# Kernel optimization log

Hardware: AMD Instinct MI355X
Metric: run time of the kernel (lower is better)

Reference implementation:

```python
import jax, jax.numpy as jnp
import numpy as np

B, T, D, H = 4, 2048, 1024, 16
HD = D // H
EPS = 1e-5
NEG = 1e10


def setup_inputs() -> dict:
    key = jax.random.key(0)
    k1, k2, k3 = jax.random.split(key, 3)
    return {
        "target": jax.random.normal(k1, (B, T, D), dtype=jnp.float32),
        "w_qkv": jax.random.normal(k2, (D, 3 * D), dtype=jnp.float32) * 0.02,
        "w_proj": jax.random.normal(k3, (D, D), dtype=jnp.float32) * (0.02 / np.sqrt(24.0)),
        "b_proj": jnp.zeros((D,), dtype=jnp.float32),
        "ln_gamma": jnp.ones((D,), dtype=jnp.float32),
        "ln_beta": jnp.zeros((D,), dtype=jnp.float32),
    }


def reference(target, w_qkv, w_proj, b_proj, ln_gamma, ln_beta):
    b, t, d = target.shape
    resid = target
    qkv = target @ w_qkv                      # [B,T,3D]
    q, k, v = jnp.split(qkv, 3, axis=-1)
    # [B,H,T,hd]
    q = q.reshape(b, t, H, HD).transpose(0, 2, 1, 3)
    k = k.reshape(b, t, H, HD).transpose(0, 2, 1, 3)
    v = v.reshape(b, t, H, HD).transpose(0, 2, 1, 3)
    scores = jnp.einsum("bhqd,bhkd->bhqk", q, k) * (1.0 / np.sqrt(HD))
    causal = (jnp.arange(t)[:, None] >= jnp.arange(t)[None, :]).astype(scores.dtype)
    scores = scores * causal - (1.0 - causal) * NEG
    attn = jax.nn.softmax(scores, axis=-1)
    out = jnp.einsum("bhqk,bhkd->bhqd", attn, v)
    out = out.transpose(0, 2, 1, 3).reshape(b, t, d)
    proj = out @ w_proj + b_proj
    x = proj + resid
    mu = jnp.mean(x, axis=-1, keepdims=True)
    var = jnp.var(x, axis=-1, keepdims=True)
    return ((x - mu) * jax.lax.rsqrt(var + EPS)) * ln_gamma + ln_beta
```

## Files before the change

kernel.cpp:

```cpp
#include <hip/hip_runtime.h>
#include <hip/hip_bf16.h>

#define Bsz 4
#define Tseq 2048
#define Dmodel 1024
#define Hn 16
#define HD 64
#define EPS 1e-5f
#define QSCALE 0.18033688011112042f

typedef __attribute__((ext_vector_type(8))) short bf16x8;
typedef __attribute__((ext_vector_type(4))) short bf16x4;
typedef __attribute__((ext_vector_type(4))) float f32x4;
typedef __attribute__((ext_vector_type(4))) unsigned short us4;
typedef __attribute__((ext_vector_type(2))) unsigned uint2v;

typedef const __attribute__((address_space(1))) void* gas_t;
typedef __attribute__((address_space(3))) void* las_t;

__device__ __forceinline__ unsigned short f2bf(float x) {
    unsigned u = __builtin_bit_cast(unsigned, x);
    u += 0x7fffu + ((u >> 16) & 1u);
    return (unsigned short)(u >> 16);
}
__device__ __forceinline__ unsigned pack2bf_t(float a, float b) {
    return __builtin_amdgcn_perm(__builtin_bit_cast(unsigned, b),
                                 __builtin_bit_cast(unsigned, a), 0x07060302u);
}

__device__ __forceinline__ float exp2_raw(float x) {
#if __has_builtin(__builtin_amdgcn_exp2f)
    return __builtin_amdgcn_exp2f(x);
#else
    float r;
    asm("v_exp_f32 %0, %1" : "=v"(r) : "v"(x));
    return r;
#endif
}

__device__ __forceinline__ f32x4 mfma16x16x16(bf16x4 a, bf16x4 b, f32x4 c) {
#if __has_builtin(__builtin_amdgcn_mfma_f32_16x16x16bf16_1k)
    return __builtin_amdgcn_mfma_f32_16x16x16bf16_1k(a, b, c, 0, 0, 0);
#else
    asm("v_mfma_f32_16x16x16_bf16 %0, %1, %2, %0" : "+v"(c) : "v"(a), "v"(b));
    return c;
#endif
}

__global__ __launch_bounds__(256)
void prep(const float* __restrict__ target, unsigned short* __restrict__ tgt_bf,
          const float* __restrict__ w_qkv, unsigned short* __restrict__ wqT,
          const float* __restrict__ w_proj, unsigned short* __restrict__ wpT) {
    const int bid = blockIdx.x;
    const int tid = threadIdx.x;
    if (bid < 8192) {
        int i = (bid * 256 + tid) * 4;
        float4 v = *(const float4*)(target + i);
        us4 o = { f2bf(v.x), f2bf(v.y), f2bf(v.z), f2bf(v.w) };
        *(us4*)(tgt_bf + i) = o;
        return;
    }
    __shared__ unsigned short t[32][33];
    const float* in;
    unsigned short* outp;
    int K = 1024, N, bx, by;
    if (bid < 8192 + 3072) {
        const int b2 = bid - 8192;
        in = w_qkv; outp = wqT; N = 3072;
        bx = b2 % 96; by = b2 / 96;
    } else {
        const int b3 = bid - 8192 - 3072;
        in = w_proj; outp = wpT; N = 1024;
        bx = b3 & 31; by = b3 >> 5;
    }
    const int k0 = by * 32, n0 = bx * 32;
    const int tx = tid & 31, ty = tid >> 5;
    #pragma unroll
    for (int i = 0; i < 32; i += 8)
        t[ty + i][tx] = f2bf(in[(size_t)(k0 + ty + i) * N + n0 + tx]);
    __syncthreads();
    #pragma unroll
    for (int i = 0; i < 32; i += 8)
        outp[(size_t)(n0 + ty + i) * K + k0 + tx] = t[tx][ty + i];
}

template<bool OUT_BF16, bool SCALEQ>
__global__ __launch_bounds__(256)
void gemm_mfma(const unsigned short* __restrict__ A,
               const unsigned short* __restrict__ Bt,
               void* __restrict__ Cv, int M, int N, int K,
               const float* __restrict__ bias, const float* __restrict__ resid) {
    __shared__ unsigned short As[2][128 * 32];
    __shared__ unsigned short Bs[2][128 * 32];
    const int tid = threadIdx.x;
    const int w = tid >> 6, lane = tid & 63;
    const int l16 = lane & 15, quad = lane >> 4;

    const int lin = blockIdx.y * gridDim.x + blockIdx.x;
    const int chunk = (gridDim.x * gridDim.y) >> 3;
    const int neff = (lin & 7) * chunk + (lin >> 3);
    const int bx = neff % gridDim.x, by = neff / gridDim.x;
    const int m0 = by * 128, n0 = bx * 128;

    f32x4 acc[4][4];
    #pragma unroll
    for (int i = 0; i < 4; ++i)
        #pragma unroll
        for (int j = 0; j < 4; ++j)
            acc[i][j] = f32x4{0.f, 0.f, 0.f, 0.f};

    const int lrow = lane >> 2, lcol = lane & 3;
    const unsigned short* ag = A  + (size_t)(m0 + w * 32 + lrow) * K + lcol * 8;
    const unsigned short* bg = Bt + (size_t)(n0 + w * 32 + lrow) * K + lcol * 8;
    unsigned short* al0 = As[0] + (w * 32) * 32;
    unsigned short* al1 = As[0] + (w * 32 + 16) * 32;
    unsigned short* ah0 = As[1] + (w * 32) * 32;
    unsigned short* ah1 = As[1] + (w * 32 + 16) * 32;
    unsigned short* bl0 = Bs[0] + (w * 32) * 32;
    unsigned short* bl1 = Bs[0] + (w * 32 + 16) * 32;
    unsigned short* bh0 = Bs[1] + (w * 32) * 32;
    unsigned short* bh1 = Bs[1] + (w * 32 + 16) * 32;
    const int am = (w >> 1) * 64, bn = (w & 1) * 64;

    for (int k0 = 0; k0 < K; k0 += 64) {
        __builtin_amdgcn_global_load_lds((gas_t)(ag + k0),               (las_t)al0, 16, 0, 0);
        __builtin_amdgcn_global_load_lds((gas_t)(ag + 16 * K + k0),      (las_t)al1, 16, 0, 0);
        __builtin_amdgcn_global_load_lds((gas_t)(ag + k0 + 32),          (las_t)ah0, 16, 0, 0);
        __builtin_amdgcn_global_load_lds((gas_t)(ag + 16 * K + k0 + 32), (las_t)ah1, 16, 0, 0);
        __builtin_amdgcn_global_load_lds((gas_t)(bg + k0),               (las_t)bl0, 16, 0, 0);
        __builtin_amdgcn_global_load_lds((gas_t)(bg + 16 * K + k0),      (las_t)bl1, 16, 0, 0);
        __builtin_amdgcn_global_load_lds((gas_t)(bg + k0 + 32),          (las_t)bh0, 16, 0, 0);
        __builtin_amdgcn_global_load_lds((gas_t)(bg + 16 * K + k0 + 32), (las_t)bh1, 16, 0, 0);
        __syncthreads();

        #pragma unroll
        for (int ks = 0; ks < 2; ++ks) {
            bf16x8 af[4], bf[4];
            #pragma unroll
            for (int i = 0; i < 4; ++i)
                af[i] = *(const bf16x8*)&As[ks][(am + i * 16 + l16) * 32 + quad * 8];
            #pragma unroll
            for (int j = 0; j < 4; ++j)
                bf[j] = *(const bf16x8*)&Bs[ks][(bn + j * 16 + l16) * 32 + quad * 8];
            #pragma unroll
            for (int i = 0; i < 4; ++i)
                #pragma unroll
                for (int j = 0; j < 4; ++j)
                    acc[i][j] = __builtin_amdgcn_mfma_f32_16x16x32_bf16(af[i], bf[j], acc[i][j], 0, 0, 0);
        }
        __syncthreads();
    }

    #pragma unroll
    for (int i = 0; i < 4; ++i) {
        #pragma unroll
        for (int j = 0; j < 4; ++j) {
            const int col = n0 + bn + j * 16 + l16;
            const float scale = (SCALEQ && col < Dmodel) ? QSCALE : 1.0f;
            #pragma unroll
            for (int r = 0; r < 4; ++r) {
                const int row = m0 + am + i * 16 + quad * 4 + r;
                if (OUT_BF16) {
                    ((unsigned short*)Cv)[(size_t)row * N + col] = f2bf(acc[i][j][r] * scale);
                } else {
                    float v = acc[i][j][r] + bias[col] + resid[(size_t)row * N + col];
                    ((float*)Cv)[(size_t)row * N + col] = v;
                }
            }
        }
    }
}

__global__ __launch_bounds__(256)
void flash_attn(const unsigned short* __restrict__ qkv, unsigned short* __restrict__ out) {
    const int lin = blockIdx.y * gridDim.x + blockIdx.x;
    const int xcd = lin & 7, local = lin >> 3;
    const int bh = xcd + 8 * (local & 7);
    const int x = local >> 3;
    const int qt_lo = x, qt_hi = (Tseq / 64 - 1) - x;
    const int h = bh & (Hn - 1), b = bh >> 4;
    const int tid = threadIdx.x;
    const int wave = tid >> 6;
    const int lane = tid & 63;
    const int l16 = lane & 15;
    const int quad = lane >> 4;

    __shared__ unsigned short Ks[2][2][64 * 32];
    __shared__ unsigned short Vs[2][64 * 64];

    const unsigned short* qrow = qkv + ((size_t)(b * Tseq + wave * 16 + l16)) * 3072 + h * HD;
    const unsigned short* qhi = qrow + (size_t)qt_hi * 64 * 3072;
    const unsigned short* qlo = qrow + (size_t)qt_lo * 64 * 3072;
    bf16x8 qh0 = *(const bf16x8*)(qhi + quad * 8);
    bf16x8 qh1 = *(const bf16x8*)(qhi + 32 + quad * 8);
    bf16x8 ql0 = *(const bf16x8*)(qlo + quad * 8);
    bf16x8 ql1 = *(const bf16x8*)(qlo + 32 + quad * 8);

    f32x4 lacc_hi = {0.f, 0.f, 0.f, 0.f}, lacc_lo = {0.f, 0.f, 0.f, 0.f};
    f32x4 ohi[4], olo[4];
    #pragma unroll
    for (int nt = 0; nt < 4; ++nt) {
        ohi[nt] = f32x4{0.f, 0.f, 0.f, 0.f};
        olo[nt] = f32x4{0.f, 0.f, 0.f, 0.f};
    }
    const bf16x4 vones = { (short)0x3F80, (short)0x3F80, (short)0x3F80, (short)0x3F80 };

    unsigned vrb[4];
    #pragma unroll
    for (int ntd = 0; ntd < 4; ++ntd) {
        const int d = ntd * 16 + l16;
        const int X = (d + (d >> 3)) & 7;
        vrb[ntd] = (unsigned)(d * 128 + (quad & 1) * 8)
                 ^ (unsigned)(X << 4) ^ (unsigned)((quad >> 1) << 4);
    }

    const unsigned short* kbase = qkv + (size_t)b * Tseq * 3072 + Dmodel + h * HD;
    const unsigned short* vbase = kbase + Dmodel;
    const unsigned short* kg = kbase + (size_t)(wave * 16 + (lane >> 2)) * 3072 + (lane & 3) * 8;
    const int vp = tid >> 3, vc = tid & 7;
    const unsigned short* vsrc = vbase + (size_t)(2 * vp) * 3072 + vc * 8;

    auto stageK = [&](int buf, size_t koff) {
        __builtin_amdgcn_global_load_lds((gas_t)(kg + koff),
                                         (las_t)&Ks[buf][0][wave * 16 * 32], 16, 0, 0);
        __builtin_amdgcn_global_load_lds((gas_t)(kg + koff + 32),
                                         (las_t)&Ks[buf][1][wave * 16 * 32], 16, 0, 0);
    };
    auto writeV = [&](int buf, const bf16x8& va, const bf16x8& vb) {
        const int kc = vp >> 2;
        const int kin = (2 * vp) & 7;
        #pragma unroll
        for (int j = 0; j < 8; ++j) {
            const int d = vc * 8 + j;
            const int pc = kc ^ ((d + (d >> 3)) & 7);
            unsigned pk = (unsigned)(unsigned short)va[j]
                        | ((unsigned)(unsigned short)vb[j] << 16);
            *(unsigned*)&Vs[buf][d * 64 + pc * 8 + kin] = pk;
        }
    };

    auto compute = [&](int buf, int q0t, const bf16x8& qf0, const bf16x8& qf1,
                       f32x4* oacc, f32x4& lacc, bool diag, int k0g) {
        __builtin_amdgcn_s_setprio(1);
        f32x4 st[4];
        #pragma unroll
        for (int nt = 0; nt < 4; ++nt) {
            f32x4 a = {0.f, 0.f, 0.f, 0.f};
            bf16x8 kf0 = *(const bf16x8*)&Ks[buf][0][(nt * 16 + l16) * 32 + quad * 8];
            a = __builtin_amdgcn_mfma_f32_16x16x32_bf16(kf0, qf0, a, 0, 0, 0);
            bf16x8 kf1 = *(const bf16x8*)&Ks[buf][1][(nt * 16 + l16) * 32 + quad * 8];
            a = __builtin_amdgcn_mfma_f32_16x16x32_bf16(kf1, qf1, a, 0, 0, 0);
            st[nt] = a;
        }
        if (diag) {
            const int qg = q0t + wave * 16 + l16;
            #pragma unroll
            for (int nt = 0; nt < 4; ++nt) {
                const int kgl = k0g + nt * 16 + quad * 4;
                #pragma unroll
                for (int r = 0; r < 4; ++r)
                    if (kgl + r > qg) st[nt][r] = -1e30f;
            }
        }
        bf16x4 pa[4];
        #pragma unroll
        for (int nt = 0; nt < 4; ++nt) {
            float p0 = exp2_raw(st[nt][0]);
            float p1 = exp2_raw(st[nt][1]);
            float p2 = exp2_raw(st[nt][2]);
            float p3 = exp2_raw(st[nt][3]);
            uint2v t;
            t.x = pack2bf_t(p0, p1);
            t.y = pack2bf_t(p2, p3);
            pa[nt] = __builtin_bit_cast(bf16x4, t);
        }
        const char* vsb = (const char*)&Vs[buf][0];
        #pragma unroll
        for (int ntk = 0; ntk < 4; ++ntk) {
            lacc = mfma16x16x16(pa[ntk], vones, lacc);
            #pragma unroll
            for (int ntd = 0; ntd < 4; ++ntd) {
                bf16x4 vf = *(const bf16x4*)(vsb + (vrb[ntd] ^ (unsigned)(ntk << 5)));
                oacc[ntd] = mfma16x16x16(pa[ntk], vf, oacc[ntd]);
            }
        }
        __builtin_amdgcn_s_setprio(0);
    };

    stageK(0, 0);
    bf16x8 va = *(const bf16x8*)(vsrc);
    bf16x8 vb = *(const bf16x8*)(vsrc + 3072);
    writeV(0, va, vb);
    __syncthreads();

    int cur = 0;
    for (int kt = 0; kt <= qt_hi; ++kt) {
        if (kt < qt_hi) {
            const size_t koff_n = (size_t)(kt + 1) * 64 * 3072;
            stageK(cur ^ 1, koff_n);
            va = *(const bf16x8*)(vsrc + koff_n);
            vb = *(const bf16x8*)(vsrc + koff_n + 3072);
        }

        compute(cur, qt_hi * 64, qh0, qh1, ohi, lacc_hi, kt == qt_hi, kt * 64);
        if (kt <= qt_lo)
            compute(cur, qt_lo * 64, ql0, ql1, olo, lacc_lo, kt == qt_lo, kt * 64);

        if (kt < qt_hi) writeV(cur ^ 1, va, vb);
        __syncthreads();
        cur ^= 1;
    }

    auto epilogue = [&](int q0t, f32x4* oacc, const f32x4& lacc) {
        float inv[4];
        #pragma unroll
        for (int r = 0; r < 4; ++r)
            inv[r] = __builtin_amdgcn_rcpf(lacc[r]);
        unsigned short* obase =
            out + ((size_t)(b * Tseq + q0t + wave * 16)) * Dmodel + h * HD;
        #pragma unroll
        for (int nt = 0; nt < 4; ++nt) {
            #pragma unroll
            for (int r = 0; r < 4; ++r) {
                int row = quad * 4 + r;
                obase[(size_t)row * Dmodel + nt * 16 + l16] = f2bf(oacc[nt][r] * inv[r]);
            }
        }
    };
    epilogue(qt_hi * 64, ohi, lacc_hi);
    epilogue(qt_lo * 64, olo, lacc_lo);
}

__global__ __launch_bounds__(256)
void ln_kernel(float* __restrict__ x, const float* __restrict__ gamma,
               const float* __restrict__ beta) {
    const int row = blockIdx.x;
    float* xr = x + (size_t)row * Dmodel;
    const int tid = threadIdx.x;
    const int wave = tid >> 6;
    __shared__ float ws[4], ws2[4];

    float4 v = *(const float4*)(xr + tid * 4);
    float s  = v.x + v.y + v.z + v.w;
    float s2 = v.x * v.x + v.y * v.y + v.z * v.z + v.w * v.w;
    #pragma unroll
    for (int off = 32; off; off >>= 1) {
        s  += __shfl_xor(s, off, 64);
        s2 += __shfl_xor(s2, off, 64);
    }
    if ((tid & 63) == 0) { ws[wave] = s; ws2[wave] = s2; }
    __syncthreads();
    s  = (ws[0] + ws[1]) + (ws[2] + ws[3]);
    s2 = (ws2[0] + ws2[1]) + (ws2[2] + ws2[3]);

    const float mu  = s * (1.0f / Dmodel);
    const float var = s2 * (1.0f / Dmodel) - mu * mu;
    const float rstd = rsqrtf(var + EPS);

    float4 g = *(const float4*)(gamma + tid * 4);
    float4 bt = *(const float4*)(beta + tid * 4);
    float4 o;
    o.x = (v.x - mu) * rstd * g.x + bt.x;
    o.y = (v.y - mu) * rstd * g.y + bt.y;
    o.z = (v.z - mu) * rstd * g.z + bt.z;
    o.w = (v.w - mu) * rstd * g.w + bt.w;
    *(float4*)(xr + tid * 4) = o;
}

extern "C" void kernel_launch(void* const* d_in, const int* in_sizes, int n_in,
                              void* d_out, int out_size, void* d_ws, size_t ws_size,
                              hipStream_t stream) {
    const float* target   = (const float*)d_in[0];
    const float* w_qkv    = (const float*)d_in[1];
    const float* w_proj   = (const float*)d_in[2];
    const float* b_proj   = (const float*)d_in[3];
    const float* ln_gamma = (const float*)d_in[4];
    const float* ln_beta  = (const float*)d_in[5];
    float* out = (float*)d_out;

    const int M = Bsz * Tseq;

    char* ws = (char*)d_ws;
    unsigned short* qkv_bf16 = (unsigned short*)(ws);
    unsigned short* attn_bf  = (unsigned short*)(ws + 48ull * 1024 * 1024);
    unsigned short* tgt_bf   = (unsigned short*)(ws + 64ull * 1024 * 1024);
    unsigned short* wqT      = (unsigned short*)(ws + 80ull * 1024 * 1024);
    unsigned short* wpT      = (unsigned short*)(ws + 86ull * 1024 * 1024);

    prep<<<dim3(8192 + 3072 + 1024), 256, 0, stream>>>(
        target, tgt_bf, w_qkv, wqT, w_proj, wpT);

    gemm_mfma<true, true><<<dim3(3072 / 128, M / 128), 256, 0, stream>>>(
        tgt_bf, wqT, qkv_bf16, M, 3072, Dmodel, nullptr, nullptr);

    flash_attn<<<dim3(16, Bsz * Hn), 256, 0, stream>>>(qkv_bf16, attn_bf);

    gemm_mfma<false, false><<<dim3(Dmodel / 128, M / 128), 256, 0, stream>>>(
        attn_bf, wpT, out, M, Dmodel, Dmodel, b_proj, target);

    ln_kernel<<<dim3(M), 256, 0, stream>>>(out, ln_gamma, ln_beta);
}
```

Before: 273.5 us.

## Fuse dual-query-tile attention compute and widen V transpose stores to 64-bit

Merges the two per-tile compute calls into one dual pass, so each K and V fragment read from LDS feeds both the high and low query tiles and their MFMAs can interleave. The V staging is reorganised so each thread loads four rows of four columns and writes 64-bit packed transposed chunks instead of eight 32-bit stores. The intent is to cut redundant LDS reads and store instructions and to raise MFMA ILP. The cost is higher register pressure from holding two sets of P fragments at once. It also assumes qt_hi is never below qt_lo, since the dual branch applies no causal mask to the high tile.

```diff
diff --git a/kernel.cpp b/kernel.cpp
--- a/kernel.cpp
+++ b/kernel.cpp
@@ -26,6 +26,11 @@
 __device__ __forceinline__ unsigned pack2bf_t(float a, float b) {
     return __builtin_amdgcn_perm(__builtin_bit_cast(unsigned, b),
                                  __builtin_bit_cast(unsigned, a), 0x07060302u);
+}
+__device__ __forceinline__ unsigned pack_sel(uint2v a, uint2v b, int j) {
+    unsigned ad = a[j >> 1], bd = b[j >> 1];
+    return (j & 1) ? __builtin_amdgcn_perm(bd, ad, 0x07060302u)
+                   : __builtin_amdgcn_perm(bd, ad, 0x05040100u);
 }
 
 __device__ __forceinline__ float exp2_raw(float x) {
@@ -217,8 +222,8 @@
     const unsigned short* kbase = qkv + (size_t)b * Tseq * 3072 + Dmodel + h * HD;
     const unsigned short* vbase = kbase + Dmodel;
     const unsigned short* kg = kbase + (size_t)(wave * 16 + (lane >> 2)) * 3072 + (lane & 3) * 8;
-    const int vp = tid >> 3, vc = tid & 7;
-    const unsigned short* vsrc = vbase + (size_t)(2 * vp) * 3072 + vc * 8;
+    const int kq = tid >> 4, dq = tid & 15;
+    const unsigned short* vsrc = vbase + (size_t)(4 * kq) * 3072 + dq * 4;
 
     auto stageK = [&](int buf, size_t koff) {
         __builtin_amdgcn_global_load_lds((gas_t)(kg + koff),
@@ -226,71 +231,86 @@
         __builtin_amdgcn_global_load_lds((gas_t)(kg + koff + 32),
                                          (las_t)&Ks[buf][1][wave * 16 * 32], 16, 0, 0);
     };
-    auto writeV = [&](int buf, const bf16x8& va, const bf16x8& vb) {
-        const int kc = vp >> 2;
-        const int kin = (2 * vp) & 7;
-        #pragma unroll
-        for (int j = 0; j < 8; ++j) {
-            const int d = vc * 8 + j;
+    auto loadV = [&](size_t koff, uint2v* v4) {
+        const unsigned short* vr = vsrc + koff;
+        v4[0] = *(const uint2v*)(vr);
+        v4[1] = *(const uint2v*)(vr + 3072);
+        v4[2] = *(const uint2v*)(vr + 2 * 3072);
+        v4[3] = *(const uint2v*)(vr + 3 * 3072);
+    };
+    auto writeV = [&](int buf, const uint2v* v4) {
+        const int kc = kq >> 1;
+        const int kin = (kq & 1) * 4;
+        #pragma unroll
+        for (int j = 0; j < 4; ++j) {
+            const int d = dq * 4 + j;
             const int pc = kc ^ ((d + (d >> 3)) & 7);
-            unsigned pk = (unsigned)(unsigned short)va[j]
-                        | ((unsigned)(unsigned short)vb[j] << 16);
-            *(unsigned*)&Vs[buf][d * 64 + pc * 8 + kin] = pk;
+            uint2v wv;
+            wv.x = pack_sel(v4[0], v4[1], j);
+            wv.y = pack_sel(v4[2], v4[3], j);
+            *(uint2v*)&Vs[buf][d * 64 + pc * 8 + kin] = wv;
         }
     };
 
-    auto compute = [&](int buf, int q0t, const bf16x8& qf0, const bf16x8& qf1,
-                       f32x4* oacc, f32x4& lacc, bool diag, int k0g) {
+    auto computeDual = [&](int buf, bool dual, bool diag_hi, bool diag_lo, int k0g)
+            __attribute__((always_inline)) {
         __builtin_amdgcn_s_setprio(1);
-        f32x4 st[4];
+        bf16x4 pah[4], pal[4];
+        const int qg_hi = qt_hi * 64 + wave * 16 + l16;
+        const int qg_lo = qt_lo * 64 + wave * 16 + l16;
         #pragma unroll
         for (int nt = 0; nt < 4; ++nt) {
-            f32x4 a = {0.f, 0.f, 0.f, 0.f};
             bf16x8 kf0 = *(const bf16x8*)&Ks[buf][0][(nt * 16 + l16) * 32 + quad * 8];
-            a = __builtin_amdgcn_mfma_f32_16x16x32_bf16(kf0, qf0, a, 0, 0, 0);
             bf16x8 kf1 = *(const bf16x8*)&Ks[buf][1][(nt * 16 + l16) * 32 + quad * 8];
-            a = __builtin_amdgcn_mfma_f32_16x16x32_bf16(kf1, qf1, a, 0, 0, 0);
-            st[nt] = a;
-        }
-        if (diag) {
-            const int qg = q0t + wave * 16 + l16;
-            #pragma unroll
-            for (int nt = 0; nt < 4; ++nt) {
-                const int kgl = k0g + nt * 16 + quad * 4;
-                #pragma unroll
-                for (int r = 0; r < 4; ++r)
-                    if (kgl + r > qg) st[nt][r] = -1e30f;
+            const int kgl = k0g + nt * 16 + quad * 4;
+            {
+                f32x4 a = {0.f, 0.f, 0.f, 0.f};
+                a = __builtin_amdgcn_mfma_f32_16x16x32_bf16(kf0, qh0, a, 0, 0, 0);
+                a = __builtin_amdgcn_mfma_f32_16x16x32_bf16(kf1, qh1, a, 0, 0, 0);
+                if (diag_hi) {
+                    #pragma unroll
+                    for (int r = 0; r < 4; ++r)
+                        if (kgl + r > qg_hi) a[r] = -1e30f;
+                }
+                uint2v t;
+                t.x = pack2bf_t(exp2_raw(a[0]), exp2_raw(a[1]));
+                t.y = pack2bf_t(exp2_raw(a[2]), exp2_raw(a[3]));
+                pah[nt] = __builtin_bit_cast(bf16x4, t);
             }
-        }
-        bf16x4 pa[4];
-        #pragma unroll
-        for (int nt = 0; nt < 4; ++nt) {
-            float p0 = exp2_raw(st[nt][0]);
-            float p1 = exp2_raw(st[nt][1]);
-            float p2 = exp2_raw(st[nt][2]);
-            float p3 = exp2_raw(st[nt][3]);
-            uint2v t;
-            t.x = pack2bf_t(p0, p1);
-            t.y = pack2bf_t(p2, p3);
-            pa[nt] = __builtin_bit_cast(bf16x4, t);
+            if (dual) {
+                f32x4 a = {0.f, 0.f, 0.f, 0.f};
+                a = __builtin_amdgcn_mfma_f32_16x16x32_bf16(kf0, ql0, a, 0, 0, 0);
+                a = __builtin_amdgcn_mfma_f32_16x16x32_bf16(kf1, ql1, a, 0, 0, 0);
+                if (diag_lo) {
+                    #pragma unroll
+                    for (int r = 0; r < 4; ++r)
+                        if (kgl + r > qg_lo) a[r] = -1e30f;
+                }
+                uint2v t;
+                t.x = pack2bf_t(exp2_raw(a[0]), exp2_raw(a[1]));
+                t.y = pack2bf_t(exp2_raw(a[2]), exp2_raw(a[3]));
+                pal[nt] = __builtin_bit_cast(bf16x4, t);
+            }
         }
         const char* vsb = (const char*)&Vs[buf][0];
         #pragma unroll
         for (int ntk = 0; ntk < 4; ++ntk) {
-            lacc = mfma16x16x16(pa[ntk], vones, lacc);
+            lacc_hi = mfma16x16x16(pah[ntk], vones, lacc_hi);
+            if (dual) lacc_lo = mfma16x16x16(pal[ntk], vones, lacc_lo);
             #pragma unroll
             for (int ntd = 0; ntd < 4; ++ntd) {
                 bf16x4 vf = *(const bf16x4*)(vsb + (vrb[ntd] ^ (unsigned)(ntk << 5)));
-                oacc[ntd] = mfma16x16x16(pa[ntk], vf, oacc[ntd]);
+                ohi[ntd] = mfma16x16x16(pah[ntk], vf, ohi[ntd]);
+                if (dual) olo[ntd] = mfma16x16x16(pal[ntk], vf, olo[ntd]);
             }
         }
         __builtin_amdgcn_s_setprio(0);
     };
 
     stageK(0, 0);
-    bf16x8 va = *(const bf16x8*)(vsrc);
-    bf16x8 vb = *(const bf16x8*)(vsrc + 3072);
-    writeV(0, va, vb);
+    uint2v v4[4];
+    loadV(0, v4);
+    writeV(0, v4);
     __syncthreads();
 
     int cur = 0;
@@ -298,15 +318,15 @@
         if (kt < qt_hi) {
             const size_t koff_n = (size_t)(kt + 1) * 64 * 3072;
             stageK(cur ^ 1, koff_n);
-            va = *(const bf16x8*)(vsrc + koff_n);
-            vb = *(const bf16x8*)(vsrc + koff_n + 3072);
-        }
-
-        compute(cur, qt_hi * 64, qh0, qh1, ohi, lacc_hi, kt == qt_hi, kt * 64);
+            loadV(koff_n, v4);
+        }
+
         if (kt <= qt_lo)
-            compute(cur, qt_lo * 64, ql0, ql1, olo, lacc_lo, kt == qt_lo, kt * 64);
-
-        if (kt < qt_hi) writeV(cur ^ 1, va, vb);
+            computeDual(cur, true, false, kt == qt_lo, kt * 64);
+        else
+            computeDual(cur, false, kt == qt_hi, false, kt * 64);
+
+        if (kt < qt_hi) writeV(cur ^ 1, v4);
         __syncthreads();
         cur ^= 1;
     }
```

Result: no change. 275.7 us (+0.8%).

## Use 128-row query tiles with 512-thread attention blocks sharing K/V loads

Applied to the files above, without the earlier changes.

The flash attention kernel now processes 128-query tiles with 8 waves per block, so each K/V tile staged into LDS is reused by twice as many query rows. The grid halves, K staging is split across waves by head-dim half, and each thread loads smaller V chunks. The tile-pair order is permuted to balance causal work across blocks. Fewer, larger blocks may reduce occupancy and load balance, and the diagonal mask handling inside the 128-row tile has to stay correct.

```diff
diff --git a/kernel.cpp b/kernel.cpp
--- a/kernel.cpp
+++ b/kernel.cpp
@@ -171,13 +171,14 @@
     }
 }
 
-__global__ __launch_bounds__(256)
+__global__ __launch_bounds__(512)
 void flash_attn(const unsigned short* __restrict__ qkv, unsigned short* __restrict__ out) {
     const int lin = blockIdx.y * gridDim.x + blockIdx.x;
     const int xcd = lin & 7, local = lin >> 3;
     const int bh = xcd + 8 * (local & 7);
-    const int x = local >> 3;
-    const int qt_lo = x, qt_hi = (Tseq / 64 - 1) - x;
+    const int q = local >> 3;
+    const int x = (q < 4) ? q : 11 - q;
+    const int tlo = x, thi = 15 - x;
     const int h = bh & (Hn - 1), b = bh >> 4;
     const int tid = threadIdx.x;
     const int wave = tid >> 6;
@@ -189,8 +190,8 @@
     __shared__ unsigned short Vs[2][64 * 64];
 
     const unsigned short* qrow = qkv + ((size_t)(b * Tseq + wave * 16 + l16)) * 3072 + h * HD;
-    const unsigned short* qhi = qrow + (size_t)qt_hi * 64 * 3072;
-    const unsigned short* qlo = qrow + (size_t)qt_lo * 64 * 3072;
+    const unsigned short* qhi = qrow + (size_t)thi * 128 * 3072;
+    const unsigned short* qlo = qrow + (size_t)tlo * 128 * 3072;
     bf16x8 qh0 = *(const bf16x8*)(qhi + quad * 8);
     bf16x8 qh1 = *(const bf16x8*)(qhi + 32 + quad * 8);
     bf16x8 ql0 = *(const bf16x8*)(qlo + quad * 8);
@@ -216,22 +217,22 @@
 
     const unsigned short* kbase = qkv + (size_t)b * Tseq * 3072 + Dmodel + h * HD;
     const unsigned short* vbase = kbase + Dmodel;
-    const unsigned short* kg = kbase + (size_t)(wave * 16 + (lane >> 2)) * 3072 + (lane & 3) * 8;
-    const int vp = tid >> 3, vc = tid & 7;
-    const unsigned short* vsrc = vbase + (size_t)(2 * vp) * 3072 + vc * 8;
+    const int khalf = wave >> 2;
+    const int krow  = (wave & 3) * 16 + (lane >> 2);
+    const unsigned short* kg = kbase + (size_t)krow * 3072 + (lane & 3) * 8 + khalf * 32;
+    const int vp = tid >> 4, vc = tid & 15;
+    const unsigned short* vsrc = vbase + (size_t)(2 * vp) * 3072 + vc * 4;
 
     auto stageK = [&](int buf, size_t koff) {
         __builtin_amdgcn_global_load_lds((gas_t)(kg + koff),
-                                         (las_t)&Ks[buf][0][wave * 16 * 32], 16, 0, 0);
-        __builtin_amdgcn_global_load_lds((gas_t)(kg + koff + 32),
-                                         (las_t)&Ks[buf][1][wave * 16 * 32], 16, 0, 0);
+                                         (las_t)&Ks[buf][khalf][(wave & 3) * 512], 16, 0, 0);
     };
-    auto writeV = [&](int buf, const bf16x8& va, const bf16x8& vb) {
+    auto writeV = [&](int buf, const bf16x4& va, const bf16x4& vb) {
         const int kc = vp >> 2;
         const int kin = (2 * vp) & 7;
         #pragma unroll
-        for (int j = 0; j < 8; ++j) {
-            const int d = vc * 8 + j;
+        for (int j = 0; j < 4; ++j) {
+            const int d = vc * 4 + j;
             const int pc = kc ^ ((d + (d >> 3)) & 7);
             unsigned pk = (unsigned)(unsigned short)va[j]
                         | ((unsigned)(unsigned short)vb[j] << 16);
@@ -287,26 +288,29 @@
         __builtin_amdgcn_s_setprio(0);
     };
 
+    const int ktmax = 31 - 2 * x;
+    const int ktlo  = 2 * x + 1;
+
     stageK(0, 0);
-    bf16x8 va = *(const bf16x8*)(vsrc);
-    bf16x8 vb = *(const bf16x8*)(vsrc + 3072);
+    bf16x4 va = *(const bf16x4*)(vsrc);
+    bf16x4 vb = *(const bf16x4*)(vsrc + 3072);
     writeV(0, va, vb);
     __syncthreads();
 
     int cur = 0;
-    for (int kt = 0; kt <= qt_hi; ++kt) {
-        if (kt < qt_hi) {
+    for (int kt = 0; kt <= ktmax; ++kt) {
+        if (kt < ktmax) {
             const size_t koff_n = (size_t)(kt + 1) * 64 * 3072;
             stageK(cur ^ 1, koff_n);
-            va = *(const bf16x8*)(vsrc + koff_n);
-            vb = *(const bf16x8*)(vsrc + koff_n + 3072);
-        }
-
-        compute(cur, qt_hi * 64, qh0, qh1, ohi, lacc_hi, kt == qt_hi, kt * 64);
-        if (kt <= qt_lo)
-            compute(cur, qt_lo * 64, ql0, ql1, olo, lacc_lo, kt == qt_lo, kt * 64);
-
-        if (kt < qt_hi) writeV(cur ^ 1, va, vb);
+            va = *(const bf16x4*)(vsrc + koff_n);
+            vb = *(const bf16x4*)(vsrc + koff_n + 3072);
+        }
+
+        compute(cur, thi * 128, qh0, qh1, ohi, lacc_hi, (kt >> 1) == thi, kt * 64);
+        if (kt <= ktlo)
+            compute(cur, tlo * 128, ql0, ql1, olo, lacc_lo, (kt >> 1) == tlo, kt * 64);
+
+        if (kt < ktmax) writeV(cur ^ 1, va, vb);
         __syncthreads();
         cur ^= 1;
     }
@@ -327,8 +331,8 @@
             }
         }
     };
-    epilogue(qt_hi * 64, ohi, lacc_hi);
-    epilogue(qt_lo * 64, olo, lacc_lo);
+    epilogue(thi * 128, ohi, lacc_hi);
+    epilogue(tlo * 128, olo, lacc_lo);
 }
 
 __global__ __launch_bounds__(256)
@@ -393,7 +397,7 @@
     gemm_mfma<true, true><<<dim3(3072 / 128, M / 128), 256, 0, stream>>>(
         tgt_bf, wqT, qkv_bf16, M, 3072, Dmodel, nullptr, nullptr);
 
-    flash_attn<<<dim3(16, Bsz * Hn), 256, 0, stream>>>(qkv_bf16, attn_bf);
+    flash_attn<<<dim3(8, Bsz * Hn), 512, 0, stream>>>(qkv_bf16, attn_bf);
 
     gemm_mfma<false, false><<<dim3(Dmodel / 128, M / 128), 256, 0, stream>>>(
         attn_bf, wpT, out, M, Dmodel, Dmodel, b_proj, target);
```

Result: no change. 276.1 us (+0.9%).
